# Performance work log

Measured on AMD Instinct MI355X. Metric: run time of the kernel, lower is better.

Reference implementation:

```python
import jax, jax.numpy as jnp
import numpy as np
import math

N_HEADS = 8
INPUT_DIM = 128
EMBED_DIM = 128
KEY_DIM = EMBED_DIM // N_HEADS  # 16, val_dim == key_dim
BATCH = 4
GRAPH = 2048


def setup_inputs() -> dict:
    key = jax.random.key(0)
    k1, k2, k3, k4, k5 = jax.random.split(key, 5)
    h = jax.random.normal(k1, (BATCH, GRAPH, INPUT_DIM), dtype=jnp.float32)
    # torch.rand -> uniform [0,1)
    W_query = jax.random.uniform(k2, (N_HEADS, INPUT_DIM, KEY_DIM), dtype=jnp.float32)
    W_key = jax.random.uniform(k3, (N_HEADS, INPUT_DIM, KEY_DIM), dtype=jnp.float32)
    W_val = jax.random.uniform(k4, (N_HEADS, INPUT_DIM, KEY_DIM), dtype=jnp.float32)
    W_out = jax.random.uniform(k5, (N_HEADS, KEY_DIM, EMBED_DIM), dtype=jnp.float32)
    return {"h": h, "W_query": W_query, "W_key": W_key, "W_val": W_val, "W_out": W_out}


def reference(h, W_query, W_key, W_val, W_out):
    # q defaults to h (self-attention)
    norm = 1.0 / math.sqrt(KEY_DIM)
    # per-head projections: [H, B, N, dk]
    Q = jnp.einsum('bnd,hdk->hbnk', h, W_query)
    K = jnp.einsum('bnd,hdk->hbnk', h, W_key)
    V = jnp.einsum('bnd,hdv->hbnv', h, W_val)
    compat = norm * jnp.einsum('hbqk,hbnk->hbqn', Q, K)  # [H, B, Nq, N]
    attn = jax.nn.softmax(compat, axis=-1)
    heads = jnp.einsum('hbqn,hbnv->hbqv', attn, V)  # [H, B, Nq, dv]
    out = jnp.einsum('hbqv,hve->bqe', heads, W_out)  # [B, Nq, E]
    return out
```

## Files before the change

kernel.cpp:

```cpp
#include <hip/hip_runtime.h>

typedef __attribute__((ext_vector_type(4))) float f32x4;
typedef __attribute__((ext_vector_type(8))) short bf16x8;

constexpr int NH = 8, D = 128, DK = 16, B = 4, N = 2048;
constexpr int KTILE = 128;
constexpr int NTILES = N / KTILE;
constexpr int TILE_SHORTS = 6144;
constexpr float QSCALE = 0.36067376022224085f;

__device__ __forceinline__ unsigned short f2bf(float f) {
    union { float f; unsigned u; } v; v.f = f;
    return (unsigned short)((v.u + 0x7fffu + ((v.u >> 16) & 1u)) >> 16);
}
__device__ __forceinline__ float bf2f(unsigned short h) {
    union { unsigned u; float f; } v; v.u = ((unsigned)h) << 16; return v.f;
}
__device__ __forceinline__ unsigned pack2(float a, float b) {
    union { float f; unsigned u; } x, y; x.f = a; y.f = b;
    return (x.u >> 16) | (y.u & 0xFFFF0000u);
}
__device__ __forceinline__ float fexp2(float x) {
    float r; asm("v_exp_f32 %0, %1" : "=v"(r) : "v"(x)); return r;
}
__device__ __forceinline__ float fmax3(float a, float b, float c) {
    float r; asm("v_max3_f32 %0, %1, %2, %3" : "=v"(r) : "v"(a), "v"(b), "v"(c));
    return r;
}

__global__ __launch_bounds__(256) void wprep_kernel(
    const float* __restrict__ Wq, const float* __restrict__ Wk,
    const float* __restrict__ Wv, const float* __restrict__ Wo,
    unsigned short* __restrict__ Wf, unsigned short* __restrict__ Wof)
{
    const int t = blockIdx.x * 256 + threadIdx.x;
    if (t < 49152) {
        const int p = t >> 14, r = t & 16383;
        const int head = r >> 11, d = (r >> 4) & 127, kk = r & 15;
        const float wv = (p == 0 ? Wq : p == 1 ? Wk : Wv)[r];
        const unsigned short hi = f2bf(wv);
        const unsigned short lo = f2bf(wv - bf2f(hi));
        const int c = p * 8 + head, s = d >> 4, dd = d & 15;
        const int ch = dd >> 3, j = dd & 7;
        Wf[((c * 8 + s) * 64 + kk + 16 * ch) * 8 + j] = hi;
        Wf[((c * 8 + s) * 64 + kk + 16 * (2 + ch)) * 8 + j] = lo;
    } else {
        const int r = t - 49152;
        const int head = r >> 11, v = (r >> 7) & 15, e = r & 127;
        const float wv = Wo[r];
        const unsigned short hi = f2bf(wv);
        const unsigned short lo = f2bf(wv - bf2f(hi));
        const int c = e >> 4, s = head, ch = v >> 3, j = v & 7;
        Wof[((c * 8 + s) * 64 + (e & 15) + 16 * ch) * 8 + j] = hi;
        Wof[((c * 8 + s) * 64 + (e & 15) + 16 * (2 + ch)) * 8 + j] = lo;
    }
}

constexpr int GR = 32;
__global__ __launch_bounds__(256) void qkv_gemm(
    const float* __restrict__ h, const unsigned short* __restrict__ Wf,
    float* __restrict__ Q, unsigned short* __restrict__ KV)
{
    const int cg = blockIdx.x % 3;
    const int row0 = (blockIdx.x / 3) * GR;
    const int b = row0 >> 11, n0 = row0 & (N - 1);
    const int t = threadIdx.x, w = t >> 6, l = t & 63;
    __shared__ unsigned short hf[8][2][64][8];

    #pragma unroll
    for (int pass = 0; pass < 4; ++pass) {
        const int rb = pass * 8 + (t >> 5);
        const int d0 = (t & 31) * 4;
        float4 hv = *(const float4*)&h[(size_t)(row0 + rb) * D + d0];
        #pragma unroll
        for (int i = 0; i < 4; ++i) {
            const int d = d0 + i;
            const float x = ((const float*)&hv)[i];
            const unsigned short hi = f2bf(x);
            const unsigned short lo = f2bf(x - bf2f(hi));
            const int s = d >> 4, dd = d & 15, ch = dd >> 3, j = dd & 7;
            hf[s][rb >> 4][(rb & 15) + 16 * ch][j] = hi;
            hf[s][rb >> 4][(rb & 15) + 16 * (2 + ch)][j] = lo;
        }
    }
    __syncthreads();

    f32x4 acc[4];
    #pragma unroll
    for (int i = 0; i < 4; ++i) acc[i] = (f32x4){0.f, 0.f, 0.f, 0.f};

    for (int s = 0; s < 8; ++s) {
        bf16x8 b1 = *(const bf16x8*)&hf[s][w & 1][l][0];
        bf16x8 b2 = *(const bf16x8*)&hf[s][w & 1][l ^ 32][0];
        #pragma unroll
        for (int ct = 0; ct < 4; ++ct) {
            const int c = cg * 8 + (w >> 1) * 4 + ct;
            bf16x8 af = *(const bf16x8*)&Wf[((c * 8 + s) * 64 + l) * 8];
            acc[ct] = __builtin_amdgcn_mfma_f32_16x16x32_bf16(af, b1, acc[ct], 0, 0, 0);
            acc[ct] = __builtin_amdgcn_mfma_f32_16x16x32_bf16(af, b2, acc[ct], 0, 0, 0);
        }
    }

    const int n = n0 + (w & 1) * 16 + (l & 15);
    const int rl = n & 127;
    const int kk0 = (l >> 4) * 4;
    #pragma unroll
    for (int ct = 0; ct < 4; ++ct) {
        const int head = (w >> 1) * 4 + ct;
        const int hb = head * B + b;
        if (cg == 0) {
            float4 o;
            o.x = acc[ct][0]; o.y = acc[ct][1]; o.z = acc[ct][2]; o.w = acc[ct][3];
            *(float4*)&Q[((size_t)hb * N + n) * DK + kk0] = o;
        } else {
            unsigned short* tb = KV + (size_t)hb * NTILES * TILE_SHORTS
                               + (size_t)(n >> 7) * TILE_SHORTS;
            if (cg == 1) {
                const int gs = kk0 >> 3, j0 = kk0 & 7;
                const int kb2 = rl >> 5, kap = rl & 31;
                const int sub = 2 * kb2 + ((kap >> 2) & 1);
                const int row16 = 4 * (kap >> 3) + (kap & 3);
                ushort4 sh, sl;
                unsigned short* shp = (unsigned short*)&sh;
                unsigned short* slp = (unsigned short*)&sl;
                #pragma unroll
                for (int r = 0; r < 4; ++r) {
                    const unsigned short hi = f2bf(acc[ct][r]);
                    shp[r] = hi;
                    slp[r] = f2bf(acc[ct][r] - bf2f(hi));
                }
                *(ushort4*)&tb[sub * 512 + (row16 + 16 * gs) * 8 + j0] = sh;
                *(ushort4*)&tb[sub * 512 + (row16 + 16 * (2 + gs)) * 8 + j0] = sl;
            } else {
                #pragma unroll
                for (int r = 0; r < 4; ++r) {
                    const int kk = kk0 + r;
                    tb[4096 + kk * 128 + ((rl >> 3) ^ (kk & 7)) * 8 + (rl & 7)]
                        = f2bf(acc[ct][r]);
                }
            }
        }
    }
}

__global__ __launch_bounds__(256, 4) void attn_kernel(
    const float* __restrict__ Q, const unsigned short* __restrict__ KV,
    float* __restrict__ Hd)
{
    const int bid = blockIdx.x;
    const int hb = (bid & 7) * 4 + ((bid >> 3) >> 5);
    const int qt = (bid >> 3) & 31;
    const int t = threadIdx.x, w = t >> 6, l = t & 63;
    const int q16 = l & 15, g = l >> 4;
    const size_t qbase = (size_t)hb * N * DK;
    const char* kvb = (const char*)(KV + (size_t)hb * NTILES * TILE_SHORTS);

    __shared__ unsigned short smem[3][TILE_SHORTS];

    const int qrow = qt * 64 + w * 16 + q16;
    bf16x8 qhi, qlo;
    {
        const float* qp = Q + qbase + (size_t)qrow * DK + (g & 1) * 8;
        float4 qa = *(const float4*)qp, qb = *(const float4*)(qp + 4);
        #pragma unroll
        for (int i = 0; i < 8; ++i) {
            const float x = (i < 4 ? ((const float*)&qa)[i] : ((const float*)&qb)[i - 4]) * QSCALE;
            const unsigned short hi = f2bf(x);
            qhi[i] = (short)hi;
            qlo[i] = (short)f2bf(x - bf2f(hi));
        }
    }
    const bf16x8 qf1 = (g < 2) ? qhi : qlo;
    const bf16x8 qf2 = (g < 2) ? qlo : qhi;

    union { unsigned u[4]; bf16x8 v; } ones;
    #pragma unroll
    for (int i = 0; i < 4; ++i) ones.u[i] = 0x3F803F80u;

    f32x4 oacc = {0.f, 0.f, 0.f, 0.f};
    f32x4 lacc = {0.f, 0.f, 0.f, 0.f};
    float m = -3.0e38f;
    unsigned pf_prev[16];

    char* b_cur = (char*)&smem[0][0];
    char* b_nxt = (char*)&smem[1][0];
    char* b_prv = (char*)&smem[2][0];

    uint4 s0, s1, s2;
    {
        const char* gt = kvb;
        s0 = *(const uint4*)(gt + t * 16);
        s1 = *(const uint4*)(gt + 4096 + t * 16);
        s2 = *(const uint4*)(gt + 8192 + t * 16);
        *(uint4*)(b_cur + t * 16) = s0;
        *(uint4*)(b_cur + 4096 + t * 16) = s1;
        *(uint4*)(b_cur + 8192 + t * 16) = s2;
        const char* g1 = kvb + 12288;
        s0 = *(const uint4*)(g1 + t * 16);
        s1 = *(const uint4*)(g1 + 4096 + t * 16);
        s2 = *(const uint4*)(g1 + 8192 + t * 16);
    }
    __syncthreads();

    for (int tile = 0; tile < NTILES; ++tile) {
        f32x4 aA[4], aB[4];
        const f32x4 z = {0.f, 0.f, 0.f, 0.f};
        __builtin_amdgcn_s_setprio(1);
        #pragma unroll
        for (int kb = 0; kb < 4; ++kb) {
            bf16x8 kA = *(const bf16x8*)(b_cur + (2 * kb) * 1024 + l * 16);
            bf16x8 kB = *(const bf16x8*)(b_cur + (2 * kb + 1) * 1024 + l * 16);
            aA[kb] = __builtin_amdgcn_mfma_f32_16x16x32_bf16(kA, qf1, z, 0, 0, 0);
            aA[kb] = __builtin_amdgcn_mfma_f32_16x16x32_bf16(kA, qf2, aA[kb], 0, 0, 0);
            aB[kb] = __builtin_amdgcn_mfma_f32_16x16x32_bf16(kB, qf1, z, 0, 0, 0);
            aB[kb] = __builtin_amdgcn_mfma_f32_16x16x32_bf16(kB, qf2, aB[kb], 0, 0, 0);
        }
        if (tile > 0) {
            #pragma unroll
            for (int kb = 0; kb < 4; ++kb) {
                union { unsigned u[4]; bf16x8 v; } pf;
                pf.u[0] = pf_prev[4 * kb + 0]; pf.u[1] = pf_prev[4 * kb + 1];
                pf.u[2] = pf_prev[4 * kb + 2]; pf.u[3] = pf_prev[4 * kb + 3];
                bf16x8 vf = *(const bf16x8*)(b_prv + 8192 + q16 * 256 + (((kb * 4 + g) ^ (q16 & 7)) * 16));
                oacc = __builtin_amdgcn_mfma_f32_16x16x32_bf16(vf, pf.v, oacc, 0, 0, 0);
                lacc = __builtin_amdgcn_mfma_f32_16x16x32_bf16(ones.v, pf.v, lacc, 0, 0, 0);
            }
        }
        __builtin_amdgcn_s_setprio(0);

        if (tile + 1 < NTILES) {
            *(uint4*)(b_nxt + t * 16) = s0;
            *(uint4*)(b_nxt + 4096 + t * 16) = s1;
            *(uint4*)(b_nxt + 8192 + t * 16) = s2;
        }
        if (tile + 2 < NTILES) {
            const char* gt = kvb + (size_t)(tile + 2) * 12288;
            s0 = *(const uint4*)(gt + t * 16);
            s1 = *(const uint4*)(gt + 4096 + t * 16);
            s2 = *(const uint4*)(gt + 8192 + t * 16);
        }

        float t0 = fmax3(fmax3(aA[0][0], aA[0][1], aA[0][2]),
                         fmax3(aA[0][3], aB[0][0], aB[0][1]), fmaxf(aB[0][2], aB[0][3]));
        float t1 = fmax3(fmax3(aA[1][0], aA[1][1], aA[1][2]),
                         fmax3(aA[1][3], aB[1][0], aB[1][1]), fmaxf(aB[1][2], aB[1][3]));
        float t2 = fmax3(fmax3(aA[2][0], aA[2][1], aA[2][2]),
                         fmax3(aA[2][3], aB[2][0], aB[2][1]), fmaxf(aB[2][2], aB[2][3]));
        float t3 = fmax3(fmax3(aA[3][0], aA[3][1], aA[3][2]),
                         fmax3(aA[3][3], aB[3][0], aB[3][1]), fmaxf(aB[3][2], aB[3][3]));
        float tm = fmaxf(fmax3(t0, t1, t2), t3);
        tm = fmaxf(tm, __shfl_xor(tm, 16));
        tm = fmaxf(tm, __shfl_xor(tm, 32));
        if (!__all(tm - m <= 8.0f)) {
            const float nm = fmaxf(m, tm);
            const float sc = fexp2(m - nm);
            m = nm;
            oacc *= sc;
            lacc *= sc;
        }
        #pragma unroll
        for (int kb = 0; kb < 4; ++kb) {
            #pragma unroll
            for (int i = 0; i < 4; ++i) {
                aA[kb][i] = fexp2(aA[kb][i] - m);
                aB[kb][i] = fexp2(aB[kb][i] - m);
            }
        }
        #pragma unroll
        for (int kb = 0; kb < 4; ++kb) {
            pf_prev[4 * kb + 0] = pack2(aA[kb][0], aA[kb][1]);
            pf_prev[4 * kb + 1] = pack2(aA[kb][2], aA[kb][3]);
            pf_prev[4 * kb + 2] = pack2(aB[kb][0], aB[kb][1]);
            pf_prev[4 * kb + 3] = pack2(aB[kb][2], aB[kb][3]);
        }

        __syncthreads();
        char* tmp = b_prv; b_prv = b_cur; b_cur = b_nxt; b_nxt = tmp;
    }

    #pragma unroll
    for (int kb = 0; kb < 4; ++kb) {
        union { unsigned u[4]; bf16x8 v; } pf;
        pf.u[0] = pf_prev[4 * kb + 0]; pf.u[1] = pf_prev[4 * kb + 1];
        pf.u[2] = pf_prev[4 * kb + 2]; pf.u[3] = pf_prev[4 * kb + 3];
        bf16x8 vf = *(const bf16x8*)(b_prv + 8192 + q16 * 256 + (((kb * 4 + g) ^ (q16 & 7)) * 16));
        oacc = __builtin_amdgcn_mfma_f32_16x16x32_bf16(vf, pf.v, oacc, 0, 0, 0);
        lacc = __builtin_amdgcn_mfma_f32_16x16x32_bf16(ones.v, pf.v, lacc, 0, 0, 0);
    }

    const float invl = 1.f / lacc[0];
    float4 o;
    o.x = oacc[0] * invl; o.y = oacc[1] * invl;
    o.z = oacc[2] * invl; o.w = oacc[3] * invl;
    *(float4*)(Hd + qbase + (size_t)qrow * DK + g * 4) = o;
}

constexpr int OGR = 16;
__global__ __launch_bounds__(256) void out_gemm(
    const float* __restrict__ Hd, const unsigned short* __restrict__ Wof,
    float* __restrict__ out)
{
    const int row0 = blockIdx.x * OGR;
    const int b = row0 >> 11, n0 = row0 & (N - 1);
    const int t = threadIdx.x, w = t >> 6, l = t & 63;
    __shared__ unsigned short hf[8][64][8];

    #pragma unroll
    for (int pass = 0; pass < 2; ++pass) {
        const int rb = pass * 8 + (t >> 5);
        const int d0 = (t & 31) * 4;
        float4 hv = *(const float4*)&Hd[((size_t)((d0 >> 4) * B + b) * N + (n0 + rb)) * DK + (d0 & 15)];
        #pragma unroll
        for (int i = 0; i < 4; ++i) {
            const int d = d0 + i;
            const float x = ((const float*)&hv)[i];
            const unsigned short hi = f2bf(x);
            const unsigned short lo = f2bf(x - bf2f(hi));
            const int s = d >> 4, dd = d & 15, ch = dd >> 3, j = dd & 7;
            hf[s][rb + 16 * ch][j] = hi;
            hf[s][rb + 16 * (2 + ch)][j] = lo;
        }
    }
    __syncthreads();

    f32x4 acc[2];
    #pragma unroll
    for (int i = 0; i < 2; ++i) acc[i] = (f32x4){0.f, 0.f, 0.f, 0.f};

    for (int s = 0; s < 8; ++s) {
        bf16x8 b1 = *(const bf16x8*)&hf[s][l][0];
        bf16x8 b2 = *(const bf16x8*)&hf[s][l ^ 32][0];
        #pragma unroll
        for (int ct = 0; ct < 2; ++ct) {
            const int c = w * 2 + ct;
            bf16x8 af = *(const bf16x8*)&Wof[((c * 8 + s) * 64 + l) * 8];
            acc[ct] = __builtin_amdgcn_mfma_f32_16x16x32_bf16(af, b1, acc[ct], 0, 0, 0);
            acc[ct] = __builtin_amdgcn_mfma_f32_16x16x32_bf16(af, b2, acc[ct], 0, 0, 0);
        }
    }

    const int n = row0 + (l & 15);
    #pragma unroll
    for (int ct = 0; ct < 2; ++ct) {
        const int c = w * 2 + ct;
        float4 o;
        o.x = acc[ct][0]; o.y = acc[ct][1]; o.z = acc[ct][2]; o.w = acc[ct][3];
        *(float4*)&out[(size_t)n * D + c * 16 + (l >> 4) * 4] = o;
    }
}

extern "C" void kernel_launch(void* const* d_in, const int* in_sizes, int n_in,
                              void* d_out, int out_size, void* d_ws, size_t ws_size,
                              hipStream_t stream) {
    const float* h  = (const float*)d_in[0];
    const float* Wq = (const float*)d_in[1];
    const float* Wk = (const float*)d_in[2];
    const float* Wv = (const float*)d_in[3];
    const float* Wo = (const float*)d_in[4];
    float* out = (float*)d_out;

    char* ws = (char*)d_ws;
    float* Q = (float*)ws;
    unsigned short* KV  = (unsigned short*)(ws + (size_t)4 * 1024 * 1024);
    unsigned short* Wf  = (unsigned short*)(ws + (size_t)10 * 1024 * 1024);
    unsigned short* Wof = (unsigned short*)(ws + (size_t)10 * 1024 * 1024 + 196608);

    wprep_kernel<<<256, 256, 0, stream>>>(Wq, Wk, Wv, Wo, Wf, Wof);
    qkv_gemm<<<(B * N / GR) * 3, 256, 0, stream>>>(h, Wf, Q, KV);
    attn_kernel<<<NH * B * 32, 256, 0, stream>>>(Q, KV, Q);
    out_gemm<<<B * N / OGR, 256, 0, stream>>>(Q, Wof, out);
}
```

Before: 61.12 us.

## Split attention over key range into two halves with merge in output GEMM

Each attention block now handles 128 query rows with 512 threads and processes only half of the key/value tiles. Partial unnormalized outputs plus the running max and sum are written to workspace, and out_gemm merges the two halves with log-sum-exp weights before projecting. The goal is to shorten each block's serial tile loop and amortize each K/V tile load over more queries. The cost is extra partial-output traffic and merge arithmetic. The max shuffle now runs only on the rescale path, and each lane's own tile max gates the rescale check.

Measured after the change: 78.87 us. 29.0% more time.

```diff
diff --git a/kernel.cpp b/kernel.cpp
--- a/kernel.cpp
+++ b/kernel.cpp
@@ -6,6 +6,8 @@
 constexpr int NH = 8, D = 128, DK = 16, B = 4, N = 2048;
 constexpr int KTILE = 128;
 constexpr int NTILES = N / KTILE;
+constexpr int NSPLIT = 2;
+constexpr int TPS = NTILES / NSPLIT;
 constexpr int TILE_SHORTS = 6144;
 constexpr float QSCALE = 0.36067376022224085f;
 
@@ -143,21 +145,25 @@
     }
 }
 
-__global__ __launch_bounds__(256, 4) void attn_kernel(
+__global__ __launch_bounds__(512, 8) void attn_kernel(
     const float* __restrict__ Q, const unsigned short* __restrict__ KV,
-    float* __restrict__ Hd)
+    float* __restrict__ Opart, float2* __restrict__ ML)
 {
     const int bid = blockIdx.x;
-    const int hb = (bid & 7) * 4 + ((bid >> 3) >> 5);
-    const int qt = (bid >> 3) & 31;
+    const int inner = bid >> 3;
+    const int hb = (bid & 7) * 4 + (inner >> 5);
+    const int rem = inner & 31;
+    const int qt = rem >> 1;
+    const int sp = rem & 1;
     const int t = threadIdx.x, w = t >> 6, l = t & 63;
     const int q16 = l & 15, g = l >> 4;
     const size_t qbase = (size_t)hb * N * DK;
-    const char* kvb = (const char*)(KV + (size_t)hb * NTILES * TILE_SHORTS);
+    const char* kvb = (const char*)(KV + (size_t)hb * NTILES * TILE_SHORTS)
+                    + (size_t)sp * TPS * 12288;
 
     __shared__ unsigned short smem[3][TILE_SHORTS];
 
-    const int qrow = qt * 64 + w * 16 + q16;
+    const int qrow = qt * 128 + w * 16 + q16;
     bf16x8 qhi, qlo;
     {
         const float* qp = Q + qbase + (size_t)qrow * DK + (g & 1) * 8;
@@ -186,23 +192,23 @@
     char* b_nxt = (char*)&smem[1][0];
     char* b_prv = (char*)&smem[2][0];
 
-    uint4 s0, s1, s2;
+    const bool kst = (t < 256);
+    const int soff0 = kst ? t * 32 : 8192 + (t - 256) * 16;
+    const int soff1 = soff0 + 16;
+
+    uint4 s0, s1;
     {
-        const char* gt = kvb;
-        s0 = *(const uint4*)(gt + t * 16);
-        s1 = *(const uint4*)(gt + 4096 + t * 16);
-        s2 = *(const uint4*)(gt + 8192 + t * 16);
-        *(uint4*)(b_cur + t * 16) = s0;
-        *(uint4*)(b_cur + 4096 + t * 16) = s1;
-        *(uint4*)(b_cur + 8192 + t * 16) = s2;
+        s0 = *(const uint4*)(kvb + soff0);
+        if (kst) s1 = *(const uint4*)(kvb + soff1);
+        *(uint4*)(b_cur + soff0) = s0;
+        if (kst) *(uint4*)(b_cur + soff1) = s1;
         const char* g1 = kvb + 12288;
-        s0 = *(const uint4*)(g1 + t * 16);
-        s1 = *(const uint4*)(g1 + 4096 + t * 16);
-        s2 = *(const uint4*)(g1 + 8192 + t * 16);
+        s0 = *(const uint4*)(g1 + soff0);
+        if (kst) s1 = *(const uint4*)(g1 + soff1);
     }
     __syncthreads();
 
-    for (int tile = 0; tile < NTILES; ++tile) {
+    for (int tile = 0; tile < TPS; ++tile) {
         f32x4 aA[4], aB[4];
         const f32x4 z = {0.f, 0.f, 0.f, 0.f};
         __builtin_amdgcn_s_setprio(1);
@@ -228,16 +234,14 @@
         }
         __builtin_amdgcn_s_setprio(0);
 
-        if (tile + 1 < NTILES) {
-            *(uint4*)(b_nxt + t * 16) = s0;
-            *(uint4*)(b_nxt + 4096 + t * 16) = s1;
-            *(uint4*)(b_nxt + 8192 + t * 16) = s2;
-        }
-        if (tile + 2 < NTILES) {
+        if (tile + 1 < TPS) {
+            *(uint4*)(b_nxt + soff0) = s0;
+            if (kst) *(uint4*)(b_nxt + soff1) = s1;
+        }
+        if (tile + 2 < TPS) {
             const char* gt = kvb + (size_t)(tile + 2) * 12288;
-            s0 = *(const uint4*)(gt + t * 16);
-            s1 = *(const uint4*)(gt + 4096 + t * 16);
-            s2 = *(const uint4*)(gt + 8192 + t * 16);
+            s0 = *(const uint4*)(gt + soff0);
+            if (kst) s1 = *(const uint4*)(gt + soff1);
         }
 
         float t0 = fmax3(fmax3(aA[0][0], aA[0][1], aA[0][2]),
@@ -248,10 +252,10 @@
                          fmax3(aA[2][3], aB[2][0], aB[2][1]), fmaxf(aB[2][2], aB[2][3]));
         float t3 = fmax3(fmax3(aA[3][0], aA[3][1], aA[3][2]),
                          fmax3(aA[3][3], aB[3][0], aB[3][1]), fmaxf(aB[3][2], aB[3][3]));
-        float tm = fmaxf(fmax3(t0, t1, t2), t3);
-        tm = fmaxf(tm, __shfl_xor(tm, 16));
-        tm = fmaxf(tm, __shfl_xor(tm, 32));
-        if (!__all(tm - m <= 8.0f)) {
+        const float tlm = fmaxf(fmax3(t0, t1, t2), t3);
+        if (!__all(tlm - m <= 8.0f)) {
+            float tm = fmaxf(tlm, __shfl_xor(tlm, 16));
+            tm = fmaxf(tm, __shfl_xor(tm, 32));
             const float nm = fmaxf(m, tm);
             const float sc = fexp2(m - nm);
             m = nm;
@@ -288,32 +292,42 @@
         lacc = __builtin_amdgcn_mfma_f32_16x16x32_bf16(ones.v, pf.v, lacc, 0, 0, 0);
     }
 
-    const float invl = 1.f / lacc[0];
     float4 o;
-    o.x = oacc[0] * invl; o.y = oacc[1] * invl;
-    o.z = oacc[2] * invl; o.w = oacc[3] * invl;
-    *(float4*)(Hd + qbase + (size_t)qrow * DK + g * 4) = o;
+    o.x = oacc[0]; o.y = oacc[1]; o.z = oacc[2]; o.w = oacc[3];
+    *(float4*)&Opart[(((size_t)sp * 32 + hb) * N + qrow) * DK + g * 4] = o;
+    if (l < 16)
+        ML[((size_t)sp * 32 + hb) * N + qrow] = make_float2(m, lacc[0]);
 }
 
 constexpr int OGR = 16;
 __global__ __launch_bounds__(256) void out_gemm(
-    const float* __restrict__ Hd, const unsigned short* __restrict__ Wof,
-    float* __restrict__ out)
+    const float* __restrict__ Opart, const float2* __restrict__ ML,
+    const unsigned short* __restrict__ Wof, float* __restrict__ out)
 {
     const int row0 = blockIdx.x * OGR;
     const int b = row0 >> 11, n0 = row0 & (N - 1);
     const int t = threadIdx.x, w = t >> 6, l = t & 63;
     __shared__ unsigned short hf[8][64][8];
+    constexpr size_t SPLITO = (size_t)32 * N * DK;
 
     #pragma unroll
     for (int pass = 0; pass < 2; ++pass) {
         const int rb = pass * 8 + (t >> 5);
         const int d0 = (t & 31) * 4;
-        float4 hv = *(const float4*)&Hd[((size_t)((d0 >> 4) * B + b) * N + (n0 + rb)) * DK + (d0 & 15)];
+        const int head = d0 >> 4, hb = head * B + b;
+        const size_t base = ((size_t)hb * N + (n0 + rb)) * DK + (d0 & 15);
+        float4 o0 = *(const float4*)&Opart[base];
+        float4 o1 = *(const float4*)&Opart[SPLITO + base];
+        const float2 ml0 = ML[(size_t)hb * N + (n0 + rb)];
+        const float2 ml1 = ML[(size_t)32 * N + (size_t)hb * N + (n0 + rb)];
+        const float M = fmaxf(ml0.x, ml1.x);
+        const float w0 = fexp2(ml0.x - M), w1 = fexp2(ml1.x - M);
+        const float inv = 1.f / (ml0.y * w0 + ml1.y * w1);
+        const float a0 = w0 * inv, a1 = w1 * inv;
         #pragma unroll
         for (int i = 0; i < 4; ++i) {
+            const float x = ((const float*)&o0)[i] * a0 + ((const float*)&o1)[i] * a1;
             const int d = d0 + i;
-            const float x = ((const float*)&hv)[i];
             const unsigned short hi = f2bf(x);
             const unsigned short lo = f2bf(x - bf2f(hi));
             const int s = d >> 4, dd = d & 15, ch = dd >> 3, j = dd & 7;
@@ -364,9 +378,11 @@
     unsigned short* KV  = (unsigned short*)(ws + (size_t)4 * 1024 * 1024);
     unsigned short* Wf  = (unsigned short*)(ws + (size_t)10 * 1024 * 1024);
     unsigned short* Wof = (unsigned short*)(ws + (size_t)10 * 1024 * 1024 + 196608);
+    float* Opart = (float*)(ws + (size_t)11 * 1024 * 1024);
+    float2* ML   = (float2*)(ws + (size_t)19 * 1024 * 1024);
 
     wprep_kernel<<<256, 256, 0, stream>>>(Wq, Wk, Wv, Wo, Wf, Wof);
     qkv_gemm<<<(B * N / GR) * 3, 256, 0, stream>>>(h, Wf, Q, KV);
-    attn_kernel<<<NH * B * 32, 256, 0, stream>>>(Q, KV, Q);
-    out_gemm<<<B * N / OGR, 256, 0, stream>>>(Q, Wof, out);
-}
+    attn_kernel<<<NH * B * 16 * NSPLIT, 512, 0, stream>>>(Q, KV, Opart, ML);
+    out_gemm<<<B * N / OGR, 256, 0, stream>>>(Opart, ML, Wof, out);
+}
```
